# Kernel optimization log

Measured on AMD Instinct MI355X. Metric: run time of the kernel, lower is better.

## Reference

```python
import jax, jax.numpy as jnp
import numpy as np

TOK, CPC, RHY = 135, 12, 8
HID, STACK, KEY, EMB = 400, 32, 300, 50
B, T = 1, 4096


def setup_inputs() -> dict:
    key = jax.random.key(0)
    ks = jax.random.split(key, 32)
    w = lambda k, shape, s=0.05: jax.random.normal(k, shape, jnp.float32) * s
    inp = {
        'xr': jax.random.randint(ks[0], (B, T), 0, RHY, dtype=jnp.int32),
        'xcpc': jax.random.randint(ks[1], (B, T), 0, CPC, dtype=jnp.int32),
        'xma': jax.random.randint(ks[2], (B, T), 0, TOK, dtype=jnp.int32),
        'emb_midi': w(ks[3], (TOK, EMB)),
        'emb_cpc': w(ks[4], (CPC, EMB)),
        'emb_rhythm': w(ks[5], (RHY, EMB)),
        # note_rnn: 2-layer LSTM, input 3*EMB=150, hidden 400 (torch gate order i,f,g,o)
        'note_Wih0': w(ks[6], (4 * HID, 3 * EMB)),
        'note_Whh0': w(ks[7], (4 * HID, HID)),
        'note_bih0': w(ks[8], (4 * HID,)),
        'note_bhh0': w(ks[9], (4 * HID,)),
        'note_Wih1': w(ks[10], (4 * HID, HID)),
        'note_Whh1': w(ks[11], (4 * HID, HID)),
        'note_bih1': w(ks[12], (4 * HID,)),
        'note_bhh1': w(ks[13], (4 * HID,)),
        'note_fcW': w(ks[14], (3 * EMB, HID)),
        'note_fcb': w(ks[15], (3 * EMB,)),
        # stack memory
        'act_W': w(ks[16], (3, HID)),
        'act_b': w(ks[17], (3,)),
        'D_param': jax.random.normal(ks[18], (1, HID), jnp.float32),
        # key_rnn: 1-layer LSTM, input HID, hidden KEY
        'key_Wih': w(ks[19], (4 * KEY, HID)),
        'key_Whh': w(ks[20], (4 * KEY, KEY)),
        'key_bih': w(ks[21], (4 * KEY,)),
        'key_bhh': w(ks[22], (4 * KEY,)),
        'key_fcW': w(ks[23], (HID, KEY)),
        'key_fcb': w(ks[24], (HID,)),
    }
    return inp


def lstm_layer(x, Wih, Whh, bih, bhh):
    # x: [B,T,I] -> outputs [B,T,H], final (h,c) [B,H]. torch gate order i,f,g,o.
    Bsz = x.shape[0]
    H = Whh.shape[1]
    xg = jnp.einsum('bti,gi->btg', x, Wih) + bih  # precompute input projections

    def step(carry, xt):  # xt: [B,4H]
        h, c = carry
        g = xt + h @ Whh.T + bhh
        i, f, gg, o = jnp.split(g, 4, axis=-1)
        c = jax.nn.sigmoid(f) * c + jax.nn.sigmoid(i) * jnp.tanh(gg)
        h = jax.nn.sigmoid(o) * jnp.tanh(c)
        return (h, c), h

    init = (jnp.zeros((Bsz, H), x.dtype), jnp.zeros((Bsz, H), x.dtype))
    (h, c), hs = jax.lax.scan(step, init, jnp.swapaxes(xg, 0, 1))
    return jnp.swapaxes(hs, 0, 1), h, c


def stack_memory(rnn_out, act_W, act_b, D_param):
    # Per-timestep push/pop/no-op gated stack; returns per-step stack snapshots.
    Bsz, Tlen, H = rnn_out.shape
    probs = jax.nn.softmax(rnn_out @ act_W.T + act_b, axis=-1)            # [B,T,3]
    push_val = jax.nn.sigmoid(jnp.einsum('oh,bth->bt', D_param, rnn_out))  # [B,T]

    def step(s, xs):  # s: [B,STACK,H]
        p, pv = xs  # p: [B,3], pv: [B]
        a = jnp.concatenate([s[:, 1:], s[:, -1:]], axis=1)    # stack[:-1]=stack[1:]
        b = jnp.concatenate([a[:, :1], a[:, :-1]], axis=1)    # stack[1:]=stack[:-1]
        top = p[:, 0:1] * pv[:, None] + p[:, 1:2] * b[:, 1] + p[:, 2:3] * b[:, 0]
        s = b.at[:, 0].set(top)
        return s, s

    init = jnp.zeros((Bsz, STACK, H), rnn_out.dtype)
    _, stacks = jax.lax.scan(step, init, (jnp.swapaxes(probs, 0, 1), push_val.T))
    return jnp.swapaxes(stacks, 0, 1)  # [B,T,STACK,H]


def reference(xr, xcpc, xma, emb_midi, emb_cpc, emb_rhythm,
              note_Wih0, note_Whh0, note_bih0, note_bhh0,
              note_Wih1, note_Whh1, note_bih1, note_bhh1,
              note_fcW, note_fcb, act_W, act_b, D_param,
              key_Wih, key_Whh, key_bih, key_bhh, key_fcW, key_fcb):
    x = jnp.concatenate([emb_midi[xma], emb_cpc[xcpc], emb_rhythm[xr]], axis=2)  # [B,T,150]
    h0, _, _ = lstm_layer(x, note_Wih0, note_Whh0, note_bih0, note_bhh0)
    rnn_out, rh, rc = lstm_layer(h0, note_Wih1, note_Whh1, note_bih1, note_bhh1)
    rtoken_pred = rnn_out @ note_fcW.T + note_fcb  # dropout is identity in eval
    context = stack_memory(rnn_out, act_W, act_b, D_param)  # [B,T,STACK,HID]
    key_in = rh[:, None, :]  # [B,1,HID] (prev_key concat dropped; see notes)
    krnn_out, kh, kc = lstm_layer(key_in, key_Wih, key_Whh, key_bih, key_bhh)
    ktoken_pred = krnn_out @ key_fcW.T + key_fcb  # [B,1,HID]
    return (rtoken_pred, ktoken_pred, context)
```

## Files before the change

### kernel.cpp

```cpp
#include <hip/hip_runtime.h>
#include <stdint.h>

#define T_LEN 4096
#define HID   400
#define G4    1600
#define KDIM  300
#define STACKN 32

__device__ __forceinline__ float fsig(float x){ return 1.f/(1.f + __expf(-x)); }
__device__ __forceinline__ float ftanh(float x){ float e = __expf(2.f*x); return 1.f - 2.f/(e+1.f); }

__global__ void __launch_bounds__(256) kgemm0(
    const int* __restrict__ xma, const int* __restrict__ xcpc, const int* __restrict__ xr,
    const float* __restrict__ em, const float* __restrict__ ec, const float* __restrict__ er,
    const float* __restrict__ W, const float* __restrict__ b1, const float* __restrict__ b2,
    float* __restrict__ XG)
{
  __shared__ float xs[8*152];
  const int t0 = blockIdx.x*8;
  const int tid = threadIdx.x;
  for (int idx = tid; idx < 8*150; idx += 256){
    int tt = idx / 150, k = idx - tt*150;
    int t = t0 + tt;
    float v;
    if (k < 50)       v = em[(size_t)xma[t]*50 + k];
    else if (k < 100) v = ec[(size_t)xcpc[t]*50 + (k-50)];
    else              v = er[(size_t)xr[t]*50 + (k-100)];
    xs[tt*152 + k] = v;
  }
  __syncthreads();
  int r = blockIdx.y*256 + tid;
  if (r >= G4) return;
  float acc[8];
  #pragma unroll
  for (int i=0;i<8;i++) acc[i]=0.f;
  const float2* wr = (const float2*)(W + (size_t)r*150);
  for (int k2=0;k2<75;k2++){
    float2 w = wr[k2];
    int k = 2*k2;
    #pragma unroll
    for (int tt=0;tt<8;tt++)
      acc[tt] += w.x*xs[tt*152+k] + w.y*xs[tt*152+k+1];
  }
  float bb = b1[r] + b2[r];
  #pragma unroll
  for (int tt=0;tt<8;tt++)
    XG[(size_t)(t0+tt)*G4 + r] = acc[tt] + bb;
}

__global__ void __launch_bounds__(512,1) kpipe(
    const float* __restrict__ XG0,
    const float* __restrict__ Whh0, const float* __restrict__ Whh1,
    const float* __restrict__ Wih1, const float* __restrict__ bih1,
    const float* __restrict__ bhh1,
    float* __restrict__ RN,
    unsigned long long* hbufA, unsigned long long* hbufB,
    unsigned long long* gbuf, int T)
{
  const int wid = blockIdx.x;
  const int tid = threadIdx.x;
  const int row_local = tid >> 2;
  const int part = tid & 3;
  const bool mat = (row_local < 100);

  __shared__ float lds_h[HID];
  __shared__ float lds_g[100];
  __shared__ float lds_xg[100];
  __shared__ float lds_hnew[25];

  if (wid < 16){
    const int w = wid;
    float wreg[100];
    if (mat){
      int gate = row_local/25, jj = row_local%25;
      int row = gate*400 + w*25 + jj;
      const float4* wr = (const float4*)(Whh0 + (size_t)row*HID) + part*25;
      #pragma unroll
      for (int i=0;i<25;i++){
        float4 v = wr[i];
        wreg[4*i]=v.x; wreg[4*i+1]=v.y; wreg[4*i+2]=v.z; wreg[4*i+3]=v.w;
      }
    }
    const bool ew = (tid < 25);
    const int j = w*25 + tid;
    float c = 0.f;
    for (int t=0; t<T; t++){
      float xgi=0.f, xgf=0.f, xgg=0.f, xgo=0.f;
      if (ew){
        const float* xrw = XG0 + (size_t)t*G4;
        xgi = xrw[j]; xgf = xrw[HID+j]; xgg = xrw[2*HID+j]; xgo = xrw[3*HID+j];
      }
      if (tid < HID){
        float hv = 0.f;
        if (t > 0){
          if (tid >= w*25 && tid < w*25+25){
            hv = lds_hnew[tid - w*25];
          } else {
            const unsigned long long* src = hbufA + (size_t)(t&3)*HID + tid;
            unsigned long long ex;
            do { ex = __hip_atomic_load(src, __ATOMIC_RELAXED, __HIP_MEMORY_SCOPE_AGENT); }
            while ((unsigned)(ex >> 32) != (unsigned)t);
            union{unsigned u; float f;} cv; cv.u = (unsigned)ex; hv = cv.f;
          }
        }
        lds_h[tid] = hv;
      }
      __syncthreads();
      float sum = 0.f;
      if (mat){
        const float4* hp = (const float4*)(lds_h + part*100);
        #pragma unroll
        for (int i=0;i<25;i++){
          float4 h4 = hp[i];
          sum += wreg[4*i]*h4.x + wreg[4*i+1]*h4.y + wreg[4*i+2]*h4.z + wreg[4*i+3]*h4.w;
        }
      }
      sum += __shfl_xor(sum, 1);
      sum += __shfl_xor(sum, 2);
      if (mat && part==0) lds_g[row_local] = sum;
      __syncthreads();
      if (ew){
        float gi = xgi + lds_g[tid];
        float gf = xgf + lds_g[25+tid];
        float gg = xgg + lds_g[50+tid];
        float go = xgo + lds_g[75+tid];
        float si = fsig(gi), sf = fsig(gf), so = fsig(go), tg = ftanh(gg);
        c = sf*c + si*tg;
        float h = so*ftanh(c);
        lds_hnew[tid] = h;
        union{unsigned u; float f;} cv; cv.f = h;
        unsigned long long pk = ((unsigned long long)(unsigned)(t+1) << 32) | (unsigned long long)cv.u;
        __hip_atomic_store(hbufA + (size_t)((t+1)&3)*HID + j, pk,
                           __ATOMIC_RELAXED, __HIP_MEMORY_SCOPE_AGENT);
      }
      __syncthreads();
    }
  } else if (wid < 32){
    const int f = wid - 16;
    float wreg[100];
    float bias = 0.f;
    int grow = 0;
    if (mat){
      int gate = row_local/25, jj = row_local%25;
      grow = gate*400 + f*25 + jj;
      const float4* wr = (const float4*)(Wih1 + (size_t)grow*HID) + part*25;
      #pragma unroll
      for (int i=0;i<25;i++){
        float4 v = wr[i];
        wreg[4*i]=v.x; wreg[4*i+1]=v.y; wreg[4*i+2]=v.z; wreg[4*i+3]=v.w;
      }
      if (part==0) bias = bih1[grow] + bhh1[grow];
    }
    for (int t=0; t<T; t++){
      if (tid < HID){
        const unsigned long long* src = hbufA + (size_t)((t+1)&3)*HID + tid;
        unsigned long long ex;
        do { ex = __hip_atomic_load(src, __ATOMIC_RELAXED, __HIP_MEMORY_SCOPE_AGENT); }
        while ((unsigned)(ex >> 32) != (unsigned)(t+1));
        union{unsigned u; float f;} cv; cv.u = (unsigned)ex;
        lds_h[tid] = cv.f;
      }
      __syncthreads();
      float sum = 0.f;
      if (mat){
        const float4* hp = (const float4*)(lds_h + part*100);
        #pragma unroll
        for (int i=0;i<25;i++){
          float4 h4 = hp[i];
          sum += wreg[4*i]*h4.x + wreg[4*i+1]*h4.y + wreg[4*i+2]*h4.z + wreg[4*i+3]*h4.w;
        }
      }
      sum += __shfl_xor(sum, 1);
      sum += __shfl_xor(sum, 2);
      if (mat && part==0){
        union{unsigned u; float f;} cv; cv.f = sum + bias;
        unsigned long long pk = ((unsigned long long)(unsigned)(t+1) << 32) | (unsigned long long)cv.u;
        __hip_atomic_store(gbuf + (size_t)((t+1)&3)*G4 + grow, pk,
                           __ATOMIC_RELAXED, __HIP_MEMORY_SCOPE_AGENT);
      }
      __syncthreads();
    }
  } else {
    const int l = wid - 32;
    float wreg[100];
    if (mat){
      int gate = row_local/25, jj = row_local%25;
      int row = gate*400 + l*25 + jj;
      const float4* wr = (const float4*)(Whh1 + (size_t)row*HID) + part*25;
      #pragma unroll
      for (int i=0;i<25;i++){
        float4 v = wr[i];
        wreg[4*i]=v.x; wreg[4*i+1]=v.y; wreg[4*i+2]=v.z; wreg[4*i+3]=v.w;
      }
    }
    const bool ew = (tid < 25);
    const int j = l*25 + tid;
    float c = 0.f;
    for (int t=0; t<T; t++){
      if (tid < HID){
        float hv = 0.f;
        if (t > 0){
          if (tid >= l*25 && tid < l*25+25){
            hv = lds_hnew[tid - l*25];
          } else {
            const unsigned long long* src = hbufB + (size_t)(t&3)*HID + tid;
            unsigned long long ex;
            do { ex = __hip_atomic_load(src, __ATOMIC_RELAXED, __HIP_MEMORY_SCOPE_AGENT); }
            while ((unsigned)(ex >> 32) != (unsigned)t);
            union{unsigned u; float f;} cv; cv.u = (unsigned)ex; hv = cv.f;
          }
        }
        lds_h[tid] = hv;
      } else if (tid < 500){
        int i = tid - 400;
        int gate = i/25, jj = i - gate*25;
        const unsigned long long* src = gbuf + (size_t)((t+1)&3)*G4 + gate*400 + l*25 + jj;
        unsigned long long ex;
        do { ex = __hip_atomic_load(src, __ATOMIC_RELAXED, __HIP_MEMORY_SCOPE_AGENT); }
        while ((unsigned)(ex >> 32) != (unsigned)(t+1));
        union{unsigned u; float f;} cv; cv.u = (unsigned)ex;
        lds_xg[i] = cv.f;
      }
      __syncthreads();
      float sum = 0.f;
      if (mat){
        const float4* hp = (const float4*)(lds_h + part*100);
        #pragma unroll
        for (int i=0;i<25;i++){
          float4 h4 = hp[i];
          sum += wreg[4*i]*h4.x + wreg[4*i+1]*h4.y + wreg[4*i+2]*h4.z + wreg[4*i+3]*h4.w;
        }
      }
      sum += __shfl_xor(sum, 1);
      sum += __shfl_xor(sum, 2);
      if (mat && part==0) lds_g[row_local] = sum;
      __syncthreads();
      if (ew){
        float gi = lds_xg[tid]    + lds_g[tid];
        float gf = lds_xg[25+tid] + lds_g[25+tid];
        float gg = lds_xg[50+tid] + lds_g[50+tid];
        float go = lds_xg[75+tid] + lds_g[75+tid];
        float si = fsig(gi), sf = fsig(gf), so = fsig(go), tg = ftanh(gg);
        c = sf*c + si*tg;
        float h = so*ftanh(c);
        lds_hnew[tid] = h;
        RN[(size_t)t*HID + j] = h;
        union{unsigned u; float f;} cv; cv.f = h;
        unsigned long long pk = ((unsigned long long)(unsigned)(t+1) << 32) | (unsigned long long)cv.u;
        __hip_atomic_store(hbufB + (size_t)((t+1)&3)*HID + j, pk,
                           __ATOMIC_RELAXED, __HIP_MEMORY_SCOPE_AGENT);
      }
      __syncthreads();
    }
  }
}

__global__ void __launch_bounds__(256) krtoken(
    const float* __restrict__ RN, const float* __restrict__ fcW,
    const float* __restrict__ fcb, float* __restrict__ out)
{
  __shared__ float xs[8*400];
  const int t0 = blockIdx.x*8;
  const int tid = threadIdx.x;
  for (int idx = tid; idx < 8*400; idx += 256)
    xs[idx] = RN[(size_t)t0*400 + idx];
  __syncthreads();
  if (tid >= 150) return;
  float acc[8];
  #pragma unroll
  for (int i=0;i<8;i++) acc[i]=0.f;
  const float4* wr = (const float4*)(fcW + (size_t)tid*400);
  for (int k4=0;k4<100;k4++){
    float4 w = wr[k4];
    #pragma unroll
    for (int tt=0;tt<8;tt++){
      const float4 x4 = *(const float4*)(xs + tt*400 + 4*k4);
      acc[tt] += w.x*x4.x + w.y*x4.y + w.z*x4.z + w.w*x4.w;
    }
  }
  float bb = fcb[tid];
  #pragma unroll
  for (int tt=0;tt<8;tt++)
    out[(size_t)(t0+tt)*150 + tid] = acc[tt] + bb;
}

__global__ void kfinal(const float* __restrict__ RN, const float* __restrict__ actW,
                       const float* __restrict__ actb, const float* __restrict__ Dp,
                       float* __restrict__ vbuf)
{
  int t = blockIdx.x, l = threadIdx.x;
  const float* r = RN + (size_t)t*HID;
  float s0=0.f, s1=0.f, s2=0.f, sd=0.f;
  for (int k=l; k<HID; k+=64){
    float rv = r[k];
    s0 += actW[k]*rv;
    s1 += actW[400+k]*rv;
    s2 += actW[800+k]*rv;
    sd += Dp[k]*rv;
  }
  #pragma unroll
  for (int o=1;o<64;o<<=1){
    s0 += __shfl_xor(s0,o); s1 += __shfl_xor(s1,o);
    s2 += __shfl_xor(s2,o); sd += __shfl_xor(sd,o);
  }
  if (l==0){
    s0 += actb[0]; s1 += actb[1]; s2 += actb[2];
    float m = fmaxf(s0, fmaxf(s1, s2));
    float e0 = __expf(s0-m), e1 = __expf(s1-m), e2 = __expf(s2-m);
    float p0 = e0/(e0+e1+e2);
    vbuf[t] = p0 * fsig(sd);
  }
}

__global__ void kctx(const float* __restrict__ vbuf, uint4* __restrict__ ctx, int n16){
  int i = blockIdx.x*256 + threadIdx.x;
  int stride = gridDim.x*256;
  for (; i<n16; i+=stride){
    int t = i / 3200;
    int p = i - t*3200;
    uint4 z;
    if (p < 100){
      float v = vbuf[t];
      union{float f; uint32_t u;} cv; cv.f = v;
      z.x = z.y = z.z = z.w = cv.u;
    } else {
      z.x = z.y = z.z = z.w = 0u;
    }
    ctx[i] = z;
  }
}

__global__ void __launch_bounds__(512) kkey(
    const float* __restrict__ RN, const float* __restrict__ Wih,
    const float* __restrict__ bih, const float* __restrict__ bhh,
    const float* __restrict__ fcW, const float* __restrict__ fcb,
    float* __restrict__ out)
{
  __shared__ float rh[HID];
  __shared__ float gk[4*KDIM];
  __shared__ float hk[KDIM];
  int tid = threadIdx.x;
  if (tid < HID) rh[tid] = RN[(size_t)(T_LEN-1)*HID + tid];
  __syncthreads();
  for (int r = tid; r < 4*KDIM; r += 512){
    const float4* wr = (const float4*)(Wih + (size_t)r*HID);
    float acc = 0.f;
    for (int k4=0;k4<100;k4++){
      float4 w = wr[k4];
      const float4 x4 = *(const float4*)(rh + 4*k4);
      acc += w.x*x4.x + w.y*x4.y + w.z*x4.z + w.w*x4.w;
    }
    gk[r] = acc + bih[r] + bhh[r];
  }
  __syncthreads();
  if (tid < KDIM){
    float gi = gk[tid], gg = gk[2*KDIM+tid], go = gk[3*KDIM+tid];
    float cc = fsig(gi)*ftanh(gg);
    hk[tid] = fsig(go)*ftanh(cc);
  }
  __syncthreads();
  if (tid < HID){
    const float4* wr = (const float4*)(fcW + (size_t)tid*KDIM);
    float acc = 0.f;
    for (int k4=0;k4<75;k4++){
      float4 w = wr[k4];
      const float4 x4 = *(const float4*)(hk + 4*k4);
      acc += w.x*x4.x + w.y*x4.y + w.z*x4.z + w.w*x4.w;
    }
    out[tid] = acc + fcb[tid];
  }
}

extern "C" void kernel_launch(void* const* d_in, const int* in_sizes, int n_in,
                              void* d_out, int out_size, void* d_ws, size_t ws_size,
                              hipStream_t stream)
{
  (void)in_sizes; (void)n_in; (void)ws_size;
  const int*   xr   = (const int*)d_in[0];
  const int*   xcpc = (const int*)d_in[1];
  const int*   xma  = (const int*)d_in[2];
  const float* em   = (const float*)d_in[3];
  const float* ec   = (const float*)d_in[4];
  const float* er   = (const float*)d_in[5];
  const float* Wih0 = (const float*)d_in[6];
  const float* Whh0 = (const float*)d_in[7];
  const float* bih0 = (const float*)d_in[8];
  const float* bhh0 = (const float*)d_in[9];
  const float* Wih1 = (const float*)d_in[10];
  const float* Whh1 = (const float*)d_in[11];
  const float* bih1 = (const float*)d_in[12];
  const float* bhh1 = (const float*)d_in[13];
  const float* fcW  = (const float*)d_in[14];
  const float* fcb  = (const float*)d_in[15];
  const float* actW = (const float*)d_in[16];
  const float* actb = (const float*)d_in[17];
  const float* Dp   = (const float*)d_in[18];
  const float* kWih = (const float*)d_in[19];
  const float* kbih = (const float*)d_in[21];
  const float* kbhh = (const float*)d_in[22];
  const float* kfcW = (const float*)d_in[23];
  const float* kfcb = (const float*)d_in[24];

  float* vbuf = (float*)d_ws;

  float* out = (float*)d_out;
  char*  ob  = (char*)d_out;
  size_t total = (size_t)out_size * 4;
  float* XG0 = (float*)(ob + total - 26214400);
  float* RN  = (float*)(ob + total - 32768000);
  char*  ctl = ob + total - 32768000 - 131072;
  unsigned long long* hbufA = (unsigned long long*)(ctl);
  unsigned long long* hbufB = (unsigned long long*)(ctl + 12800);
  unsigned long long* gbuf  = (unsigned long long*)(ctl + 25600);

  float* rtok = out;
  float* ktok = out + 614400;
  uint4* ctxp = (uint4*)(ob + 614800u*4u);
  int n16 = (int)((total - 614800u*4u) >> 4);

  dim3 gg(T_LEN/8, 7);
  kgemm0<<<gg,256,0,stream>>>(xma, xcpc, xr, em, ec, er, Wih0, bih0, bhh0, XG0);
  kpipe<<<48,512,0,stream>>>(XG0, Whh0, Whh1, Wih1, bih1, bhh1, RN,
                             hbufA, hbufB, gbuf, T_LEN);
  krtoken<<<T_LEN/8,256,0,stream>>>(RN, fcW, fcb, rtok);
  kkey<<<1,512,0,stream>>>(RN, kWih, kbih, kbhh, kfcW, kfcb, ktok);
  kfinal<<<T_LEN,64,0,stream>>>(RN, actW, actb, Dp, vbuf);
  kctx<<<2048,256,0,stream>>>(vbuf, ctxp, n16);
}
```

Baseline: 8.147 ms.

## Deepen LSTM pipeline ring buffers with progress-based backpressure and wave-split dot products

Widens the tagged h/gate ring buffers from 4 to 8 slots. It adds explicit per-block progress counters so producers wait on consumer progress, and the input-projection blocks no longer need a trailing barrier each step. The mat-vec partitioning changes from 4 adjacent lanes with shuffle reduction to one K-quarter per wave, with partial sums reduced through LDS. The goal is to let the layer-1 input-projection stage run further ahead and to cut per-step synchronisation on the serial recurrence. It adds progress polling traffic and an extra LDS reduction step.

New measurement: 11.39 ms. 1.4x slower.

```diff
diff --git a/kernel.cpp b/kernel.cpp
--- a/kernel.cpp
+++ b/kernel.cpp
@@ -9,6 +9,26 @@
 
 __device__ __forceinline__ float fsig(float x){ return 1.f/(1.f + __expf(-x)); }
 __device__ __forceinline__ float ftanh(float x){ float e = __expf(2.f*x); return 1.f - 2.f/(e+1.f); }
+
+__device__ __forceinline__ float wait_tag(const unsigned long long* p, unsigned want){
+  unsigned long long ex;
+  do { ex = __hip_atomic_load(p, __ATOMIC_RELAXED, __HIP_MEMORY_SCOPE_AGENT); }
+  while ((unsigned)(ex >> 32) != want);
+  union{unsigned u; float f;} c; c.u = (unsigned)ex; return c.f;
+}
+__device__ __forceinline__ void pub_tag(unsigned long long* p, unsigned tag, float v){
+  union{unsigned u; float f;} c; c.f = v;
+  __hip_atomic_store(p, ((unsigned long long)tag << 32) | (unsigned long long)c.u,
+                     __ATOMIC_RELAXED, __HIP_MEMORY_SCOPE_AGENT);
+}
+__device__ __forceinline__ void wait_ge(const unsigned* p, unsigned want){
+  while (__hip_atomic_load(p, __ATOMIC_RELAXED, __HIP_MEMORY_SCOPE_AGENT) < want) {}
+}
+__device__ __forceinline__ void set_prog(unsigned* p, unsigned v){
+  __hip_atomic_store(p, v, __ATOMIC_RELAXED, __HIP_MEMORY_SCOPE_AGENT);
+}
+
+__global__ void kinit(unsigned* p){ p[threadIdx.x] = 0u; }
 
 __global__ void __launch_bounds__(256) kgemm0(
     const int* __restrict__ xma, const int* __restrict__ xcpc, const int* __restrict__ xr,
@@ -55,200 +75,163 @@
     const float* __restrict__ bhh1,
     float* __restrict__ RN,
     unsigned long long* hbufA, unsigned long long* hbufB,
-    unsigned long long* gbuf, int T)
-{
-  const int wid = blockIdx.x;
-  const int tid = threadIdx.x;
-  const int row_local = tid >> 2;
-  const int part = tid & 3;
-  const bool mat = (row_local < 100);
-
-  __shared__ float lds_h[HID];
-  __shared__ float lds_g[100];
+    unsigned long long* gbuf, unsigned* ffp, unsigned* l1p, int T)
+{
+  const int wid  = blockIdx.x;
+  const int tid  = threadIdx.x;
+  const int wave = tid >> 6;
+  const int lane = tid & 63;
+  const int part = wave & 3;
+  const int mrow = (wave>>2)*50 + lane;
+  const bool domat = (lane < 50);
+
+  __shared__ float lds_h[400];
+  __shared__ float lds_part[400];
   __shared__ float lds_xg[100];
   __shared__ float lds_hnew[25];
 
   if (wid < 16){
     const int w = wid;
-    float wreg[100];
-    if (mat){
-      int gate = row_local/25, jj = row_local%25;
-      int row = gate*400 + w*25 + jj;
-      const float4* wr = (const float4*)(Whh0 + (size_t)row*HID) + part*25;
+    float4 w4[25];
+    if (domat){
+      int gate = mrow/25, jj = mrow%25;
+      const float4* wr = (const float4*)(Whh0 + (size_t)(gate*400 + w*25 + jj)*HID) + part*25;
       #pragma unroll
-      for (int i=0;i<25;i++){
-        float4 v = wr[i];
-        wreg[4*i]=v.x; wreg[4*i+1]=v.y; wreg[4*i+2]=v.z; wreg[4*i+3]=v.w;
-      }
-    }
-    const bool ew = (tid < 25);
+      for (int i=0;i<25;i++) w4[i] = wr[i];
+    }
     const int j = w*25 + tid;
     float c = 0.f;
     for (int t=0; t<T; t++){
-      float xgi=0.f, xgf=0.f, xgg=0.f, xgo=0.f;
-      if (ew){
+      float xgi=0,xgf=0,xgg=0,xgo=0;
+      if (tid < 25){
         const float* xrw = XG0 + (size_t)t*G4;
-        xgi = xrw[j]; xgf = xrw[HID+j]; xgg = xrw[2*HID+j]; xgo = xrw[3*HID+j];
-      }
-      if (tid < HID){
+        xgi=xrw[j]; xgf=xrw[400+j]; xgg=xrw[800+j]; xgo=xrw[1200+j];
+      }
+      if (tid >= 400 && tid < 416){
+        wait_ge(&ffp[tid-400], (unsigned)(t>=7 ? t-7 : 0));
+      }
+      if (tid < 400){
         float hv = 0.f;
         if (t > 0){
-          if (tid >= w*25 && tid < w*25+25){
-            hv = lds_hnew[tid - w*25];
-          } else {
-            const unsigned long long* src = hbufA + (size_t)(t&3)*HID + tid;
-            unsigned long long ex;
-            do { ex = __hip_atomic_load(src, __ATOMIC_RELAXED, __HIP_MEMORY_SCOPE_AGENT); }
-            while ((unsigned)(ex >> 32) != (unsigned)t);
-            union{unsigned u; float f;} cv; cv.u = (unsigned)ex; hv = cv.f;
-          }
+          if (tid >= w*25 && tid < w*25+25) hv = lds_hnew[tid - w*25];
+          else hv = wait_tag(hbufA + (size_t)(t&7)*HID + tid, (unsigned)t);
         }
         lds_h[tid] = hv;
       }
       __syncthreads();
-      float sum = 0.f;
-      if (mat){
+      if (domat){
         const float4* hp = (const float4*)(lds_h + part*100);
+        float sum = 0.f;
         #pragma unroll
         for (int i=0;i<25;i++){
           float4 h4 = hp[i];
-          sum += wreg[4*i]*h4.x + wreg[4*i+1]*h4.y + wreg[4*i+2]*h4.z + wreg[4*i+3]*h4.w;
+          sum += w4[i].x*h4.x + w4[i].y*h4.y + w4[i].z*h4.z + w4[i].w*h4.w;
         }
-      }
-      sum += __shfl_xor(sum, 1);
-      sum += __shfl_xor(sum, 2);
-      if (mat && part==0) lds_g[row_local] = sum;
-      __syncthreads();
-      if (ew){
-        float gi = xgi + lds_g[tid];
-        float gf = xgf + lds_g[25+tid];
-        float gg = xgg + lds_g[50+tid];
-        float go = xgo + lds_g[75+tid];
-        float si = fsig(gi), sf = fsig(gf), so = fsig(go), tg = ftanh(gg);
-        c = sf*c + si*tg;
-        float h = so*ftanh(c);
+        lds_part[part*100 + mrow] = sum;
+      }
+      __syncthreads();
+      if (tid < 25){
+        float s0 = lds_part[tid]    + lds_part[100+tid] + lds_part[200+tid] + lds_part[300+tid];
+        float s1 = lds_part[25+tid] + lds_part[125+tid] + lds_part[225+tid] + lds_part[325+tid];
+        float s2 = lds_part[50+tid] + lds_part[150+tid] + lds_part[250+tid] + lds_part[350+tid];
+        float s3 = lds_part[75+tid] + lds_part[175+tid] + lds_part[275+tid] + lds_part[375+tid];
+        float gi = xgi+s0, gf = xgf+s1, gg = xgg+s2, go = xgo+s3;
+        c = fsig(gf)*c + fsig(gi)*ftanh(gg);
+        float h = fsig(go)*ftanh(c);
+        pub_tag(hbufA + (size_t)((t+1)&7)*HID + j, (unsigned)(t+1), h);
         lds_hnew[tid] = h;
-        union{unsigned u; float f;} cv; cv.f = h;
-        unsigned long long pk = ((unsigned long long)(unsigned)(t+1) << 32) | (unsigned long long)cv.u;
-        __hip_atomic_store(hbufA + (size_t)((t+1)&3)*HID + j, pk,
-                           __ATOMIC_RELAXED, __HIP_MEMORY_SCOPE_AGENT);
       }
       __syncthreads();
     }
   } else if (wid < 32){
     const int f = wid - 16;
-    float wreg[100];
-    float bias = 0.f;
-    int grow = 0;
-    if (mat){
-      int gate = row_local/25, jj = row_local%25;
-      grow = gate*400 + f*25 + jj;
-      const float4* wr = (const float4*)(Wih1 + (size_t)grow*HID) + part*25;
+    float4 w4[25];
+    if (domat){
+      int gate = mrow/25, jj = mrow%25;
+      const float4* wr = (const float4*)(Wih1 + (size_t)(gate*400 + f*25 + jj)*HID) + part*25;
       #pragma unroll
-      for (int i=0;i<25;i++){
-        float4 v = wr[i];
-        wreg[4*i]=v.x; wreg[4*i+1]=v.y; wreg[4*i+2]=v.z; wreg[4*i+3]=v.w;
-      }
-      if (part==0) bias = bih1[grow] + bhh1[grow];
+      for (int i=0;i<25;i++) w4[i] = wr[i];
+    }
+    float bias = 0.f; int grow = 0;
+    if (tid < 100){
+      grow = (tid/25)*400 + f*25 + (tid%25);
+      bias = bih1[grow] + bhh1[grow];
     }
     for (int t=0; t<T; t++){
-      if (tid < HID){
-        const unsigned long long* src = hbufA + (size_t)((t+1)&3)*HID + tid;
-        unsigned long long ex;
-        do { ex = __hip_atomic_load(src, __ATOMIC_RELAXED, __HIP_MEMORY_SCOPE_AGENT); }
-        while ((unsigned)(ex >> 32) != (unsigned)(t+1));
-        union{unsigned u; float f;} cv; cv.u = (unsigned)ex;
-        lds_h[tid] = cv.f;
-      }
-      __syncthreads();
-      float sum = 0.f;
-      if (mat){
+      if (tid == 400){
+        wait_ge(&l1p[f], (unsigned)(t>=7 ? t-7 : 0));
+      }
+      if (tid < 400)
+        lds_h[tid] = wait_tag(hbufA + (size_t)((t+1)&7)*HID + tid, (unsigned)(t+1));
+      __syncthreads();
+      if (tid == 400) set_prog(&ffp[f], (unsigned)(t+1));
+      if (domat){
         const float4* hp = (const float4*)(lds_h + part*100);
+        float sum = 0.f;
         #pragma unroll
         for (int i=0;i<25;i++){
           float4 h4 = hp[i];
-          sum += wreg[4*i]*h4.x + wreg[4*i+1]*h4.y + wreg[4*i+2]*h4.z + wreg[4*i+3]*h4.w;
+          sum += w4[i].x*h4.x + w4[i].y*h4.y + w4[i].z*h4.z + w4[i].w*h4.w;
         }
-      }
-      sum += __shfl_xor(sum, 1);
-      sum += __shfl_xor(sum, 2);
-      if (mat && part==0){
-        union{unsigned u; float f;} cv; cv.f = sum + bias;
-        unsigned long long pk = ((unsigned long long)(unsigned)(t+1) << 32) | (unsigned long long)cv.u;
-        __hip_atomic_store(gbuf + (size_t)((t+1)&3)*G4 + grow, pk,
-                           __ATOMIC_RELAXED, __HIP_MEMORY_SCOPE_AGENT);
-      }
-      __syncthreads();
+        lds_part[part*100 + mrow] = sum;
+      }
+      __syncthreads();
+      if (tid < 100){
+        float s = lds_part[tid] + lds_part[100+tid] + lds_part[200+tid] + lds_part[300+tid];
+        pub_tag(gbuf + (size_t)((t+1)&7)*G4 + grow, (unsigned)(t+1), s + bias);
+      }
     }
   } else {
     const int l = wid - 32;
-    float wreg[100];
-    if (mat){
-      int gate = row_local/25, jj = row_local%25;
-      int row = gate*400 + l*25 + jj;
-      const float4* wr = (const float4*)(Whh1 + (size_t)row*HID) + part*25;
+    float4 w4[25];
+    if (domat){
+      int gate = mrow/25, jj = mrow%25;
+      const float4* wr = (const float4*)(Whh1 + (size_t)(gate*400 + l*25 + jj)*HID) + part*25;
       #pragma unroll
-      for (int i=0;i<25;i++){
-        float4 v = wr[i];
-        wreg[4*i]=v.x; wreg[4*i+1]=v.y; wreg[4*i+2]=v.z; wreg[4*i+3]=v.w;
-      }
-    }
-    const bool ew = (tid < 25);
+      for (int i=0;i<25;i++) w4[i] = wr[i];
+    }
     const int j = l*25 + tid;
     float c = 0.f;
     for (int t=0; t<T; t++){
-      if (tid < HID){
+      if (tid < 400){
         float hv = 0.f;
         if (t > 0){
-          if (tid >= l*25 && tid < l*25+25){
-            hv = lds_hnew[tid - l*25];
-          } else {
-            const unsigned long long* src = hbufB + (size_t)(t&3)*HID + tid;
-            unsigned long long ex;
-            do { ex = __hip_atomic_load(src, __ATOMIC_RELAXED, __HIP_MEMORY_SCOPE_AGENT); }
-            while ((unsigned)(ex >> 32) != (unsigned)t);
-            union{unsigned u; float f;} cv; cv.u = (unsigned)ex; hv = cv.f;
-          }
+          if (tid >= l*25 && tid < l*25+25) hv = lds_hnew[tid - l*25];
+          else hv = wait_tag(hbufB + (size_t)(t&7)*HID + tid, (unsigned)t);
         }
         lds_h[tid] = hv;
       } else if (tid < 500){
-        int i = tid - 400;
-        int gate = i/25, jj = i - gate*25;
-        const unsigned long long* src = gbuf + (size_t)((t+1)&3)*G4 + gate*400 + l*25 + jj;
-        unsigned long long ex;
-        do { ex = __hip_atomic_load(src, __ATOMIC_RELAXED, __HIP_MEMORY_SCOPE_AGENT); }
-        while ((unsigned)(ex >> 32) != (unsigned)(t+1));
-        union{unsigned u; float f;} cv; cv.u = (unsigned)ex;
-        lds_xg[i] = cv.f;
-      }
-      __syncthreads();
-      float sum = 0.f;
-      if (mat){
+        int x = tid - 400;
+        int xgrow = (x/25)*400 + l*25 + (x%25);
+        lds_xg[x] = wait_tag(gbuf + (size_t)((t+1)&7)*G4 + xgrow, (unsigned)(t+1));
+      }
+      __syncthreads();
+      if (tid == 500) set_prog(&l1p[l], (unsigned)(t+1));
+      if (domat){
         const float4* hp = (const float4*)(lds_h + part*100);
+        float sum = 0.f;
         #pragma unroll
         for (int i=0;i<25;i++){
           float4 h4 = hp[i];
-          sum += wreg[4*i]*h4.x + wreg[4*i+1]*h4.y + wreg[4*i+2]*h4.z + wreg[4*i+3]*h4.w;
+          sum += w4[i].x*h4.x + w4[i].y*h4.y + w4[i].z*h4.z + w4[i].w*h4.w;
         }
-      }
-      sum += __shfl_xor(sum, 1);
-      sum += __shfl_xor(sum, 2);
-      if (mat && part==0) lds_g[row_local] = sum;
-      __syncthreads();
-      if (ew){
-        float gi = lds_xg[tid]    + lds_g[tid];
-        float gf = lds_xg[25+tid] + lds_g[25+tid];
-        float gg = lds_xg[50+tid] + lds_g[50+tid];
-        float go = lds_xg[75+tid] + lds_g[75+tid];
-        float si = fsig(gi), sf = fsig(gf), so = fsig(go), tg = ftanh(gg);
-        c = sf*c + si*tg;
-        float h = so*ftanh(c);
+        lds_part[part*100 + mrow] = sum;
+      }
+      __syncthreads();
+      if (tid < 25){
+        float s0 = lds_part[tid]    + lds_part[100+tid] + lds_part[200+tid] + lds_part[300+tid];
+        float s1 = lds_part[25+tid] + lds_part[125+tid] + lds_part[225+tid] + lds_part[325+tid];
+        float s2 = lds_part[50+tid] + lds_part[150+tid] + lds_part[250+tid] + lds_part[350+tid];
+        float s3 = lds_part[75+tid] + lds_part[175+tid] + lds_part[275+tid] + lds_part[375+tid];
+        float gi = lds_xg[tid]    + s0;
+        float gf = lds_xg[25+tid] + s1;
+        float gg = lds_xg[50+tid] + s2;
+        float go = lds_xg[75+tid] + s3;
+        c = fsig(gf)*c + fsig(gi)*ftanh(gg);
+        float h = fsig(go)*ftanh(c);
+        RN[(size_t)t*HID + j] = h;
+        pub_tag(hbufB + (size_t)((t+1)&7)*HID + j, (unsigned)(t+1), h);
         lds_hnew[tid] = h;
-        RN[(size_t)t*HID + j] = h;
-        union{unsigned u; float f;} cv; cv.f = h;
-        unsigned long long pk = ((unsigned long long)(unsigned)(t+1) << 32) | (unsigned long long)cv.u;
-        __hip_atomic_store(hbufB + (size_t)((t+1)&3)*HID + j, pk,
-                           __ATOMIC_RELAXED, __HIP_MEMORY_SCOPE_AGENT);
       }
       __syncthreads();
     }
@@ -408,10 +391,12 @@
   size_t total = (size_t)out_size * 4;
   float* XG0 = (float*)(ob + total - 26214400);
   float* RN  = (float*)(ob + total - 32768000);
-  char*  ctl = ob + total - 32768000 - 131072;
+  char*  ctl = ob + total - 32768000 - 262144;
   unsigned long long* hbufA = (unsigned long long*)(ctl);
-  unsigned long long* hbufB = (unsigned long long*)(ctl + 12800);
-  unsigned long long* gbuf  = (unsigned long long*)(ctl + 25600);
+  unsigned long long* hbufB = (unsigned long long*)(ctl + 25600);
+  unsigned long long* gbuf  = (unsigned long long*)(ctl + 51200);
+  unsigned* ffp = (unsigned*)(ctl + 153600);
+  unsigned* l1p = (unsigned*)(ctl + 153664);
 
   float* rtok = out;
   float* ktok = out + 614400;
@@ -420,8 +405,9 @@
 
   dim3 gg(T_LEN/8, 7);
   kgemm0<<<gg,256,0,stream>>>(xma, xcpc, xr, em, ec, er, Wih0, bih0, bhh0, XG0);
+  kinit<<<1,64,0,stream>>>(ffp);
   kpipe<<<48,512,0,stream>>>(XG0, Whh0, Whh1, Wih1, bih1, bhh1, RN,
-                             hbufA, hbufB, gbuf, T_LEN);
+                             hbufA, hbufB, gbuf, ffp, l1p, T_LEN);
   krtoken<<<T_LEN/8,256,0,stream>>>(RN, fcW, fcb, rtok);
   kkey<<<1,512,0,stream>>>(RN, kWih, kbih, kbhh, kfcW, kfcb, ktok);
   kfinal<<<T_LEN,64,0,stream>>>(RN, actW, actb, Dp, vbuf);
```
